# Kernel tuning notes

Hardware: AMD Instinct MI355X
Metric: run time of the kernel (lower is better)

Reference implementation:

```python
import jax, jax.numpy as jnp
import numpy as np

B, IN_DIM, D, C = 16384, 1024, 256, 100


def setup_inputs() -> dict:
    key = jax.random.key(0)
    k1, k2, k3, k4 = jax.random.split(key, 4)
    x = jax.random.normal(k1, (B, IN_DIM), dtype=jnp.float32)
    W = jax.random.normal(k2, (IN_DIM, D), dtype=jnp.float32) * (1.0 / np.sqrt(IN_DIM))
    b = jax.random.normal(k3, (D,), dtype=jnp.float32) * 0.01
    P = jax.random.normal(k4, (C, D), dtype=jnp.float32)  # class prototypes [C, D]
    return {"x": x, "W": W, "b": b, "P": P}


def reference(x, W, b, P):
    # Encoder: Z = x @ W + b  -> [B, D]
    Z = x @ W + b
    d = Z.shape[-1]
    # MSE(r, p) = mean((r - p)^2) = (|r|^2 - 2 r.p + |p|^2) / D
    # Computed via expansion to avoid the [B, C, D] broadcast intermediate.
    sq = (
        jnp.sum(Z * Z, axis=-1, keepdims=True)      # [B, 1]
        - 2.0 * (Z @ P.T)                            # [B, C]
        + jnp.sum(P * P, axis=-1)[None, :]           # [1, C]
    )
    return -sq / d  # [B, C]
```

## Files before the change

### kernel.cpp

```cpp
#include <hip/hip_runtime.h>

#define BATCH 16384
#define KDIM  1024
#define DDIM  256
#define CNUM  100
#define CPAD  112

typedef __bf16 bf16x4 __attribute__((ext_vector_type(4)));
typedef __bf16 bf16x8 __attribute__((ext_vector_type(8)));
typedef float  floatx4 __attribute__((ext_vector_type(4)));

static __device__ __forceinline__ unsigned short f2b(float f) {
    return __builtin_bit_cast(unsigned short, (__bf16)f);
}

__global__ __launch_bounds__(256) void prep_w(const float* __restrict__ W,
                                              unsigned short* __restrict__ Wt) {
    __shared__ float T[32][33];
    const int bid = blockIdx.x;
    const int k0 = (bid & 31) * 32;
    const int n0 = (bid >> 5) * 32;
    const int j  = threadIdx.x & 31;
    const int i0 = threadIdx.x >> 5;
#pragma unroll
    for (int l = 0; l < 4; ++l) {
        int i = i0 + l * 8;
        T[i][j] = W[(k0 + i) * DDIM + n0 + j];
    }
    __syncthreads();
#pragma unroll
    for (int l = 0; l < 4; ++l) {
        int i = i0 + l * 8;
        Wt[(n0 + i) * KDIM + k0 + j] = f2b(T[j][i]);
    }
}

__global__ __launch_bounds__(64) void prep_p(const float* __restrict__ P,
                                             unsigned short* __restrict__ Pbf,
                                             float* __restrict__ pnorm2) {
    const int c = blockIdx.x;
    const int lane = threadIdx.x;
    float s = 0.f;
#pragma unroll
    for (int jj = 0; jj < 4; ++jj) {
        int d = jj * 64 + lane;
        float v = (c < CNUM) ? P[c * DDIM + d] : 0.f;
        Pbf[c * DDIM + d] = f2b(v);
        s += v * v;
    }
#pragma unroll
    for (int m = 1; m < 64; m <<= 1) s += __shfl_xor(s, m, 64);
    if (lane == 0) pnorm2[c] = s;
}

__global__ __launch_bounds__(512) void fused_main(
    const float* __restrict__ x, const float* __restrict__ bias,
    const unsigned short* __restrict__ Wt, const unsigned short* __restrict__ Pbf,
    const float* __restrict__ pnorm2, float* __restrict__ out)
{
    __shared__ unsigned short As[64 * 40];
    __shared__ unsigned short Bs[256 * 40];
    __shared__ unsigned short Zs[64 * 264];
    __shared__ float rn2[2][64];

    const int tid  = threadIdx.x;
    const int wave = tid >> 6;
    const int lane = tid & 63;
    const int lm   = lane & 15;
    const int lq   = lane >> 4;
    const int rg   = wave >> 1;
    const int ch   = wave & 1;
    const int r0   = blockIdx.x * 64;

    const int rowA = tid >> 3;
    const int kcA  = (tid & 7) * 4;
    const int nB   = tid >> 1;
    const int kb0  = (tid & 1) * 16;

    const float* gA = x + (r0 + rowA) * KDIM + kcA;
    const unsigned short* gB = Wt + nB * KDIM;

    floatx4 acc[8];
#pragma unroll
    for (int f = 0; f < 8; ++f) { acc[f][0]=0.f; acc[f][1]=0.f; acc[f][2]=0.f; acc[f][3]=0.f; }

    floatx4 pa = *(const floatx4*)(gA);
    bf16x8 pb0 = *(const bf16x8*)(gB + kb0);
    bf16x8 pb1 = *(const bf16x8*)(gB + kb0 + 8);

    for (int kk = 0; kk < KDIM; kk += 32) {
        __syncthreads();
        bf16x4 ha;
        ha[0] = (__bf16)pa[0]; ha[1] = (__bf16)pa[1];
        ha[2] = (__bf16)pa[2]; ha[3] = (__bf16)pa[3];
        *(bf16x4*)&As[rowA * 40 + kcA] = ha;
        *(bf16x8*)&Bs[nB * 40 + kb0]     = pb0;
        *(bf16x8*)&Bs[nB * 40 + kb0 + 8] = pb1;
        __syncthreads();
        if (kk + 32 < KDIM) {
            pa  = *(const floatx4*)(gA + kk + 32);
            pb0 = *(const bf16x8*)(gB + kk + 32 + kb0);
            pb1 = *(const bf16x8*)(gB + kk + 32 + kb0 + 8);
        }
        bf16x8 af = *(const bf16x8*)&As[(rg * 16 + lm) * 40 + lq * 8];
#pragma unroll
        for (int f = 0; f < 8; ++f) {
            bf16x8 bfr = *(const bf16x8*)&Bs[(ch * 128 + f * 16 + lm) * 40 + lq * 8];
            acc[f] = __builtin_amdgcn_mfma_f32_16x16x32_bf16(af, bfr, acc[f], 0, 0, 0);
        }
    }

#pragma unroll
    for (int f = 0; f < 8; ++f) {
        float bb = bias[ch * 128 + f * 16 + lm];
#pragma unroll
        for (int r = 0; r < 4; ++r) acc[f][r] += bb;
    }

    float s0 = 0.f, s1 = 0.f, s2 = 0.f, s3 = 0.f;
#pragma unroll
    for (int f = 0; f < 8; ++f) {
        s0 += acc[f][0] * acc[f][0];
        s1 += acc[f][1] * acc[f][1];
        s2 += acc[f][2] * acc[f][2];
        s3 += acc[f][3] * acc[f][3];
    }
#pragma unroll
    for (int m = 1; m < 16; m <<= 1) {
        s0 += __shfl_xor(s0, m, 64);
        s1 += __shfl_xor(s1, m, 64);
        s2 += __shfl_xor(s2, m, 64);
        s3 += __shfl_xor(s3, m, 64);
    }
    if (lm == 0) {
        int rl = rg * 16 + lq * 4;
        rn2[ch][rl + 0] = s0;
        rn2[ch][rl + 1] = s1;
        rn2[ch][rl + 2] = s2;
        rn2[ch][rl + 3] = s3;
    }

#pragma unroll
    for (int f = 0; f < 8; ++f) {
        int col = ch * 128 + f * 16 + lm;
#pragma unroll
        for (int r = 0; r < 4; ++r)
            Zs[(rg * 16 + lq * 4 + r) * 264 + col] = f2b(acc[f][r]);
    }
    __syncthreads();

    if (wave < 7) {
        floatx4 acc2[4];
#pragma unroll
        for (int nf = 0; nf < 4; ++nf) { acc2[nf][0]=0.f; acc2[nf][1]=0.f; acc2[nf][2]=0.f; acc2[nf][3]=0.f; }
        const unsigned short* gP = Pbf + (wave * 16 + lm) * DDIM + lq * 8;
#pragma unroll
        for (int ks = 0; ks < 8; ++ks) {
            bf16x8 ap = *(const bf16x8*)(gP + ks * 32);
#pragma unroll
            for (int nf = 0; nf < 4; ++nf) {
                bf16x8 bz = *(const bf16x8*)&Zs[(nf * 16 + lm) * 264 + ks * 32 + lq * 8];
                acc2[nf] = __builtin_amdgcn_mfma_f32_16x16x32_bf16(ap, bz, acc2[nf], 0, 0, 0);
            }
        }
        int c0 = wave * 16 + lq * 4;
        if (c0 < CNUM) {
            floatx4 pn = *(const floatx4*)(pnorm2 + c0);
#pragma unroll
            for (int nf = 0; nf < 4; ++nf) {
                int rl = nf * 16 + lm;
                float rn = rn2[0][rl] + rn2[1][rl];
                floatx4 o;
#pragma unroll
                for (int r = 0; r < 4; ++r)
                    o[r] = (2.f * acc2[nf][r] - rn - pn[r]) * (1.f / 256.f);
                *(floatx4*)&out[(r0 + rl) * CNUM + c0] = o;
            }
        }
    }
}

extern "C" void kernel_launch(void* const* d_in, const int* in_sizes, int n_in,
                              void* d_out, int out_size, void* d_ws, size_t ws_size,
                              hipStream_t stream) {
    const float* x = (const float*)d_in[0];
    const float* W = (const float*)d_in[1];
    const float* b = (const float*)d_in[2];
    const float* P = (const float*)d_in[3];
    float* out = (float*)d_out;

    unsigned short* Wt  = (unsigned short*)d_ws;
    unsigned short* Pbf = Wt + KDIM * DDIM;
    float* pn2 = (float*)(Pbf + CPAD * DDIM);

    prep_w<<<256, 256, 0, stream>>>(W, Wt);
    prep_p<<<CPAD, 64, 0, stream>>>(P, Pbf, pn2);
    fused_main<<<BATCH / 64, 512, 0, stream>>>(x, b, Wt, Pbf, pn2, out);
}
```

Before: 136.6 us.

## Shrink row tile, load W tiles directly to LDS, alias Z buffer, merge prep kernels

Halves the rows per block to 32 with 256 threads, doubling the grid and capping launch bounds to allow more resident blocks. W tiles are now copied straight into LDS with global_load_lds instead of being staged through registers. Z aliases the A/B staging buffers to cut LDS use, and the two prep kernels are merged into one launch. The cost is that W traffic per output row doubles with the smaller tile. The unpadded 32-element LDS stride may also cause bank conflicts, and W is no longer prefetched a stage ahead.

```diff
diff --git a/kernel.cpp b/kernel.cpp
--- a/kernel.cpp
+++ b/kernel.cpp
@@ -14,54 +14,64 @@
     return __builtin_bit_cast(unsigned short, (__bf16)f);
 }
 
-__global__ __launch_bounds__(256) void prep_w(const float* __restrict__ W,
-                                              unsigned short* __restrict__ Wt) {
+static __device__ __forceinline__ void gload_lds16(const unsigned short* g,
+                                                   unsigned short* l) {
+    __builtin_amdgcn_global_load_lds(
+        (const __attribute__((address_space(1))) unsigned int*)g,
+        (__attribute__((address_space(3))) unsigned int*)l, 16, 0, 0);
+}
+
+__global__ __launch_bounds__(256) void prep(const float* __restrict__ W,
+                                            const float* __restrict__ P,
+                                            unsigned short* __restrict__ Wt,
+                                            unsigned short* __restrict__ Pbf,
+                                            float* __restrict__ pnorm2) {
     __shared__ float T[32][33];
     const int bid = blockIdx.x;
-    const int k0 = (bid & 31) * 32;
-    const int n0 = (bid >> 5) * 32;
-    const int j  = threadIdx.x & 31;
-    const int i0 = threadIdx.x >> 5;
-#pragma unroll
-    for (int l = 0; l < 4; ++l) {
-        int i = i0 + l * 8;
-        T[i][j] = W[(k0 + i) * DDIM + n0 + j];
-    }
-    __syncthreads();
-#pragma unroll
-    for (int l = 0; l < 4; ++l) {
-        int i = i0 + l * 8;
-        Wt[(n0 + i) * KDIM + k0 + j] = f2b(T[j][i]);
-    }
-}
-
-__global__ __launch_bounds__(64) void prep_p(const float* __restrict__ P,
-                                             unsigned short* __restrict__ Pbf,
-                                             float* __restrict__ pnorm2) {
-    const int c = blockIdx.x;
-    const int lane = threadIdx.x;
-    float s = 0.f;
-#pragma unroll
-    for (int jj = 0; jj < 4; ++jj) {
-        int d = jj * 64 + lane;
-        float v = (c < CNUM) ? P[c * DDIM + d] : 0.f;
-        Pbf[c * DDIM + d] = f2b(v);
-        s += v * v;
-    }
-#pragma unroll
-    for (int m = 1; m < 64; m <<= 1) s += __shfl_xor(s, m, 64);
-    if (lane == 0) pnorm2[c] = s;
-}
-
-__global__ __launch_bounds__(512) void fused_main(
+    if (bid < 256) {
+        const int k0 = (bid & 31) * 32;
+        const int n0 = (bid >> 5) * 32;
+        const int j  = threadIdx.x & 31;
+        const int i0 = threadIdx.x >> 5;
+#pragma unroll
+        for (int l = 0; l < 4; ++l) {
+            int i = i0 + l * 8;
+            T[i][j] = W[(k0 + i) * DDIM + n0 + j];
+        }
+        __syncthreads();
+#pragma unroll
+        for (int l = 0; l < 4; ++l) {
+            int i = i0 + l * 8;
+            Wt[(n0 + i) * KDIM + k0 + j] = f2b(T[j][i]);
+        }
+    } else {
+        const int wave = threadIdx.x >> 6;
+        const int lane = threadIdx.x & 63;
+        const int c = (bid - 256) * 4 + wave;
+        float s = 0.f;
+#pragma unroll
+        for (int jj = 0; jj < 4; ++jj) {
+            int d = jj * 64 + lane;
+            float v = (c < CNUM) ? P[c * DDIM + d] : 0.f;
+            Pbf[c * DDIM + d] = f2b(v);
+            s += v * v;
+        }
+#pragma unroll
+        for (int m = 1; m < 64; m <<= 1) s += __shfl_xor(s, m, 64);
+        if (lane == 0) pnorm2[c] = s;
+    }
+}
+
+__global__ __launch_bounds__(256, 8) void fused_main(
     const float* __restrict__ x, const float* __restrict__ bias,
     const unsigned short* __restrict__ Wt, const unsigned short* __restrict__ Pbf,
     const float* __restrict__ pnorm2, float* __restrict__ out)
 {
-    __shared__ unsigned short As[64 * 40];
-    __shared__ unsigned short Bs[256 * 40];
-    __shared__ unsigned short Zs[64 * 264];
-    __shared__ float rn2[2][64];
+    __shared__ unsigned short U[9216];
+    unsigned short* As = U;
+    unsigned short* Bs = U + 1024;
+    unsigned short* Zs = U;
+    __shared__ float rn2[2][32];
 
     const int tid  = threadIdx.x;
     const int wave = tid >> 6;
@@ -70,42 +80,36 @@
     const int lq   = lane >> 4;
     const int rg   = wave >> 1;
     const int ch   = wave & 1;
-    const int r0   = blockIdx.x * 64;
+    const int r0   = blockIdx.x * 32;
 
     const int rowA = tid >> 3;
     const int kcA  = (tid & 7) * 4;
-    const int nB   = tid >> 1;
-    const int kb0  = (tid & 1) * 16;
-
     const float* gA = x + (r0 + rowA) * KDIM + kcA;
-    const unsigned short* gB = Wt + nB * KDIM;
+
+    const unsigned short* gBbase = Wt + (wave * 64 + (lane >> 2)) * KDIM + (lane & 3) * 8;
 
     floatx4 acc[8];
 #pragma unroll
     for (int f = 0; f < 8; ++f) { acc[f][0]=0.f; acc[f][1]=0.f; acc[f][2]=0.f; acc[f][3]=0.f; }
 
-    floatx4 pa = *(const floatx4*)(gA);
-    bf16x8 pb0 = *(const bf16x8*)(gB + kb0);
-    bf16x8 pb1 = *(const bf16x8*)(gB + kb0 + 8);
+    floatx4 pa = *(const floatx4*)gA;
 
     for (int kk = 0; kk < KDIM; kk += 32) {
         __syncthreads();
+#pragma unroll
+        for (int c = 0; c < 4; ++c)
+            gload_lds16(gBbase + (c * 16) * KDIM + kk, Bs + (wave * 4 + c) * 512);
         bf16x4 ha;
         ha[0] = (__bf16)pa[0]; ha[1] = (__bf16)pa[1];
         ha[2] = (__bf16)pa[2]; ha[3] = (__bf16)pa[3];
-        *(bf16x4*)&As[rowA * 40 + kcA] = ha;
-        *(bf16x8*)&Bs[nB * 40 + kb0]     = pb0;
-        *(bf16x8*)&Bs[nB * 40 + kb0 + 8] = pb1;
+        *(bf16x4*)&As[rowA * 32 + kcA] = ha;
         __syncthreads();
-        if (kk + 32 < KDIM) {
-            pa  = *(const floatx4*)(gA + kk + 32);
-            pb0 = *(const bf16x8*)(gB + kk + 32 + kb0);
-            pb1 = *(const bf16x8*)(gB + kk + 32 + kb0 + 8);
-        }
-        bf16x8 af = *(const bf16x8*)&As[(rg * 16 + lm) * 40 + lq * 8];
+        bf16x8 af = *(const bf16x8*)&As[(rg * 16 + lm) * 32 + lq * 8];
+        if (kk + 32 < KDIM)
+            pa = *(const floatx4*)(gA + kk + 32);
 #pragma unroll
         for (int f = 0; f < 8; ++f) {
-            bf16x8 bfr = *(const bf16x8*)&Bs[(ch * 128 + f * 16 + lm) * 40 + lq * 8];
+            bf16x8 bfr = *(const bf16x8*)&Bs[(ch * 128 + f * 16 + lm) * 32 + lq * 8];
             acc[f] = __builtin_amdgcn_mfma_f32_16x16x32_bf16(af, bfr, acc[f], 0, 0, 0);
         }
     }
@@ -140,6 +144,8 @@
         rn2[ch][rl + 3] = s3;
     }
 
+    __syncthreads();
+
 #pragma unroll
     for (int f = 0; f < 8; ++f) {
         int col = ch * 128 + f * 16 + lm;
@@ -149,32 +155,36 @@
     }
     __syncthreads();
 
-    if (wave < 7) {
-        floatx4 acc2[4];
-#pragma unroll
-        for (int nf = 0; nf < 4; ++nf) { acc2[nf][0]=0.f; acc2[nf][1]=0.f; acc2[nf][2]=0.f; acc2[nf][3]=0.f; }
-        const unsigned short* gP = Pbf + (wave * 16 + lm) * DDIM + lq * 8;
-#pragma unroll
-        for (int ks = 0; ks < 8; ++ks) {
-            bf16x8 ap = *(const bf16x8*)(gP + ks * 32);
-#pragma unroll
-            for (int nf = 0; nf < 4; ++nf) {
-                bf16x8 bz = *(const bf16x8*)&Zs[(nf * 16 + lm) * 264 + ks * 32 + lq * 8];
-                acc2[nf] = __builtin_amdgcn_mfma_f32_16x16x32_bf16(ap, bz, acc2[nf], 0, 0, 0);
+#pragma unroll
+    for (int t = 0; t < 2; ++t) {
+        const int ct = wave * 2 + t;
+        if (ct < 7) {
+            floatx4 acc2[2];
+#pragma unroll
+            for (int nf = 0; nf < 2; ++nf) { acc2[nf][0]=0.f; acc2[nf][1]=0.f; acc2[nf][2]=0.f; acc2[nf][3]=0.f; }
+            const unsigned short* gP = Pbf + (ct * 16 + lm) * DDIM + lq * 8;
+#pragma unroll
+            for (int ks = 0; ks < 8; ++ks) {
+                bf16x8 ap = *(const bf16x8*)(gP + ks * 32);
+#pragma unroll
+                for (int nf = 0; nf < 2; ++nf) {
+                    bf16x8 bz = *(const bf16x8*)&Zs[(nf * 16 + lm) * 264 + ks * 32 + lq * 8];
+                    acc2[nf] = __builtin_amdgcn_mfma_f32_16x16x32_bf16(ap, bz, acc2[nf], 0, 0, 0);
+                }
             }
-        }
-        int c0 = wave * 16 + lq * 4;
-        if (c0 < CNUM) {
-            floatx4 pn = *(const floatx4*)(pnorm2 + c0);
-#pragma unroll
-            for (int nf = 0; nf < 4; ++nf) {
-                int rl = nf * 16 + lm;
-                float rn = rn2[0][rl] + rn2[1][rl];
-                floatx4 o;
-#pragma unroll
-                for (int r = 0; r < 4; ++r)
-                    o[r] = (2.f * acc2[nf][r] - rn - pn[r]) * (1.f / 256.f);
-                *(floatx4*)&out[(r0 + rl) * CNUM + c0] = o;
+            int c0 = ct * 16 + lq * 4;
+            if (c0 < CNUM) {
+                floatx4 pn = *(const floatx4*)(pnorm2 + c0);
+#pragma unroll
+                for (int nf = 0; nf < 2; ++nf) {
+                    int rl = nf * 16 + lm;
+                    float rn = rn2[0][rl] + rn2[1][rl];
+                    floatx4 o;
+#pragma unroll
+                    for (int r = 0; r < 4; ++r)
+                        o[r] = (2.f * acc2[nf][r] - rn - pn[r]) * (1.f / 256.f);
+                    *(floatx4*)&out[(r0 + rl) * CNUM + c0] = o;
+                }
             }
         }
     }
@@ -193,7 +203,6 @@
     unsigned short* Pbf = Wt + KDIM * DDIM;
     float* pn2 = (float*)(Pbf + CPAD * DDIM);
 
-    prep_w<<<256, 256, 0, stream>>>(W, Wt);
-    prep_p<<<CPAD, 64, 0, stream>>>(P, Pbf, pn2);
-    fused_main<<<BATCH / 64, 512, 0, stream>>>(x, b, Wt, Pbf, pn2, out);
-}
+    prep<<<256 + CPAD / 4, 256, 0, stream>>>(W, P, Wt, Pbf, pn2);
+    fused_main<<<BATCH / 32, 256, 0, stream>>>(x, b, Wt, Pbf, pn2, out);
+}
```

Result: no change. 134.1 us (-1.8%).

## Load GEMM operands directly into registers, widen block to 16 waves, merge prep kernels

Applied to the files above, without the earlier changes.

The first GEMM no longer stages x and Wt tiles through shared memory. Each wave loads its MFMA fragments straight from global memory into registers with one-step prefetching, which removes two barriers per k-step. The block grows to 1024 threads (16 waves, each covering a 16x64 output tile), and the row-norm reduction now sums four partials. The two prep kernels are merged into one launch. In exchange, Wt fragments are reread by every block without LDS reuse, global loads become narrow strided 16-byte accesses, and large blocks may limit occupancy.

```diff
diff --git a/kernel.cpp b/kernel.cpp
--- a/kernel.cpp
+++ b/kernel.cpp
@@ -14,112 +14,112 @@
     return __builtin_bit_cast(unsigned short, (__bf16)f);
 }
 
-__global__ __launch_bounds__(256) void prep_w(const float* __restrict__ W,
-                                              unsigned short* __restrict__ Wt) {
+__global__ __launch_bounds__(256) void prep(const float* __restrict__ W,
+                                            const float* __restrict__ P,
+                                            unsigned short* __restrict__ Wt,
+                                            unsigned short* __restrict__ Pbf,
+                                            float* __restrict__ pnorm2) {
     __shared__ float T[32][33];
     const int bid = blockIdx.x;
-    const int k0 = (bid & 31) * 32;
-    const int n0 = (bid >> 5) * 32;
-    const int j  = threadIdx.x & 31;
-    const int i0 = threadIdx.x >> 5;
+    if (bid < 256) {
+        const int k0 = (bid & 31) * 32;
+        const int n0 = (bid >> 5) * 32;
+        const int j  = threadIdx.x & 31;
+        const int i0 = threadIdx.x >> 5;
 #pragma unroll
-    for (int l = 0; l < 4; ++l) {
-        int i = i0 + l * 8;
-        T[i][j] = W[(k0 + i) * DDIM + n0 + j];
-    }
-    __syncthreads();
+        for (int l = 0; l < 4; ++l) {
+            int i = i0 + l * 8;
+            T[i][j] = W[(k0 + i) * DDIM + n0 + j];
+        }
+        __syncthreads();
 #pragma unroll
-    for (int l = 0; l < 4; ++l) {
-        int i = i0 + l * 8;
-        Wt[(n0 + i) * KDIM + k0 + j] = f2b(T[j][i]);
+        for (int l = 0; l < 4; ++l) {
+            int i = i0 + l * 8;
+            Wt[(n0 + i) * KDIM + k0 + j] = f2b(T[j][i]);
+        }
+    } else {
+        const int wave = threadIdx.x >> 6;
+        const int lane = threadIdx.x & 63;
+        const int c = (bid - 256) * 4 + wave;
+        float s = 0.f;
+#pragma unroll
+        for (int jj = 0; jj < 4; ++jj) {
+            int d = jj * 64 + lane;
+            float v = (c < CNUM) ? P[c * DDIM + d] : 0.f;
+            Pbf[c * DDIM + d] = f2b(v);
+            s += v * v;
+        }
+#pragma unroll
+        for (int m = 1; m < 64; m <<= 1) s += __shfl_xor(s, m, 64);
+        if (lane == 0) pnorm2[c] = s;
     }
 }
 
-__global__ __launch_bounds__(64) void prep_p(const float* __restrict__ P,
-                                             unsigned short* __restrict__ Pbf,
-                                             float* __restrict__ pnorm2) {
-    const int c = blockIdx.x;
-    const int lane = threadIdx.x;
-    float s = 0.f;
-#pragma unroll
-    for (int jj = 0; jj < 4; ++jj) {
-        int d = jj * 64 + lane;
-        float v = (c < CNUM) ? P[c * DDIM + d] : 0.f;
-        Pbf[c * DDIM + d] = f2b(v);
-        s += v * v;
-    }
-#pragma unroll
-    for (int m = 1; m < 64; m <<= 1) s += __shfl_xor(s, m, 64);
-    if (lane == 0) pnorm2[c] = s;
-}
-
-__global__ __launch_bounds__(512) void fused_main(
+__global__ __launch_bounds__(1024, 4) void fused_main(
     const float* __restrict__ x, const float* __restrict__ bias,
     const unsigned short* __restrict__ Wt, const unsigned short* __restrict__ Pbf,
     const float* __restrict__ pnorm2, float* __restrict__ out)
 {
-    __shared__ unsigned short As[64 * 40];
-    __shared__ unsigned short Bs[256 * 40];
     __shared__ unsigned short Zs[64 * 264];
-    __shared__ float rn2[2][64];
+    __shared__ float rn2[4][64];
 
     const int tid  = threadIdx.x;
     const int wave = tid >> 6;
     const int lane = tid & 63;
     const int lm   = lane & 15;
     const int lq   = lane >> 4;
-    const int rg   = wave >> 1;
-    const int ch   = wave & 1;
+    const int rc   = wave & 3;
+    const int cc   = wave >> 2;
     const int r0   = blockIdx.x * 64;
 
-    const int rowA = tid >> 3;
-    const int kcA  = (tid & 7) * 4;
-    const int nB   = tid >> 1;
-    const int kb0  = (tid & 1) * 16;
+    const float* gA = x + (r0 + rc * 16 + lm) * KDIM + lq * 8;
+    const unsigned short* gB = Wt + (cc * 64 + lm) * KDIM + lq * 8;
 
-    const float* gA = x + (r0 + rowA) * KDIM + kcA;
-    const unsigned short* gB = Wt + nB * KDIM;
+    floatx4 acc[4];
+#pragma unroll
+    for (int f = 0; f < 4; ++f) { acc[f][0]=0.f; acc[f][1]=0.f; acc[f][2]=0.f; acc[f][3]=0.f; }
 
-    floatx4 acc[8];
+    floatx4 a0 = *(const floatx4*)(gA);
+    floatx4 a1 = *(const floatx4*)(gA + 4);
+    bf16x8 bfr[4];
 #pragma unroll
-    for (int f = 0; f < 8; ++f) { acc[f][0]=0.f; acc[f][1]=0.f; acc[f][2]=0.f; acc[f][3]=0.f; }
+    for (int f = 0; f < 4; ++f)
+        bfr[f] = *(const bf16x8*)(gB + f * 16 * KDIM);
 
-    floatx4 pa = *(const floatx4*)(gA);
-    bf16x8 pb0 = *(const bf16x8*)(gB + kb0);
-    bf16x8 pb1 = *(const bf16x8*)(gB + kb0 + 8);
-
+#pragma unroll 2
     for (int kk = 0; kk < KDIM; kk += 32) {
-        __syncthreads();
-        bf16x4 ha;
-        ha[0] = (__bf16)pa[0]; ha[1] = (__bf16)pa[1];
-        ha[2] = (__bf16)pa[2]; ha[3] = (__bf16)pa[3];
-        *(bf16x4*)&As[rowA * 40 + kcA] = ha;
-        *(bf16x8*)&Bs[nB * 40 + kb0]     = pb0;
-        *(bf16x8*)&Bs[nB * 40 + kb0 + 8] = pb1;
-        __syncthreads();
+        floatx4 na0, na1;
+        bf16x8 nb[4];
         if (kk + 32 < KDIM) {
-            pa  = *(const floatx4*)(gA + kk + 32);
-            pb0 = *(const bf16x8*)(gB + kk + 32 + kb0);
-            pb1 = *(const bf16x8*)(gB + kk + 32 + kb0 + 8);
+            na0 = *(const floatx4*)(gA + kk + 32);
+            na1 = *(const floatx4*)(gA + kk + 36);
+#pragma unroll
+            for (int f = 0; f < 4; ++f)
+                nb[f] = *(const bf16x8*)(gB + f * 16 * KDIM + kk + 32);
         }
-        bf16x8 af = *(const bf16x8*)&As[(rg * 16 + lm) * 40 + lq * 8];
+        bf16x8 af;
+        af[0] = (__bf16)a0[0]; af[1] = (__bf16)a0[1];
+        af[2] = (__bf16)a0[2]; af[3] = (__bf16)a0[3];
+        af[4] = (__bf16)a1[0]; af[5] = (__bf16)a1[1];
+        af[6] = (__bf16)a1[2]; af[7] = (__bf16)a1[3];
 #pragma unroll
-        for (int f = 0; f < 8; ++f) {
-            bf16x8 bfr = *(const bf16x8*)&Bs[(ch * 128 + f * 16 + lm) * 40 + lq * 8];
-            acc[f] = __builtin_amdgcn_mfma_f32_16x16x32_bf16(af, bfr, acc[f], 0, 0, 0);
-        }
+        for (int f = 0; f < 4; ++f)
+            acc[f] = __builtin_amdgcn_mfma_f32_16x16x32_bf16(af, bfr[f], acc[f], 0, 0, 0);
+        a0 = na0; a1 = na1;
+#pragma unroll
+        for (int f = 0; f < 4; ++f) bfr[f] = nb[f];
     }
 
 #pragma unroll
-    for (int f = 0; f < 8; ++f) {
-        float bb = bias[ch * 128 + f * 16 + lm];
+    for (int f = 0; f < 4; ++f) {
+        float bb = bias[cc * 64 + f * 16 + lm];
 #pragma unroll
         for (int r = 0; r < 4; ++r) acc[f][r] += bb;
     }
 
     float s0 = 0.f, s1 = 0.f, s2 = 0.f, s3 = 0.f;
 #pragma unroll
-    for (int f = 0; f < 8; ++f) {
+    for (int f = 0; f < 4; ++f) {
         s0 += acc[f][0] * acc[f][0];
         s1 += acc[f][1] * acc[f][1];
         s2 += acc[f][2] * acc[f][2];
@@ -133,19 +133,19 @@
         s3 += __shfl_xor(s3, m, 64);
     }
     if (lm == 0) {
-        int rl = rg * 16 + lq * 4;
-        rn2[ch][rl + 0] = s0;
-        rn2[ch][rl + 1] = s1;
-        rn2[ch][rl + 2] = s2;
-        rn2[ch][rl + 3] = s3;
+        int rl = rc * 16 + lq * 4;
+        rn2[cc][rl + 0] = s0;
+        rn2[cc][rl + 1] = s1;
+        rn2[cc][rl + 2] = s2;
+        rn2[cc][rl + 3] = s3;
     }
 
 #pragma unroll
-    for (int f = 0; f < 8; ++f) {
-        int col = ch * 128 + f * 16 + lm;
+    for (int f = 0; f < 4; ++f) {
+        int col = cc * 64 + f * 16 + lm;
 #pragma unroll
         for (int r = 0; r < 4; ++r)
-            Zs[(rg * 16 + lq * 4 + r) * 264 + col] = f2b(acc[f][r]);
+            Zs[(rc * 16 + lq * 4 + r) * 264 + col] = f2b(acc[f][r]);
     }
     __syncthreads();
 
@@ -169,7 +169,7 @@
 #pragma unroll
             for (int nf = 0; nf < 4; ++nf) {
                 int rl = nf * 16 + lm;
-                float rn = rn2[0][rl] + rn2[1][rl];
+                float rn = rn2[0][rl] + rn2[1][rl] + rn2[2][rl] + rn2[3][rl];
                 floatx4 o;
 #pragma unroll
                 for (int r = 0; r < 4; ++r)
@@ -193,7 +193,6 @@
     unsigned short* Pbf = Wt + KDIM * DDIM;
     float* pn2 = (float*)(Pbf + CPAD * DDIM);
 
-    prep_w<<<256, 256, 0, stream>>>(W, Wt);
-    prep_p<<<CPAD, 64, 0, stream>>>(P, Pbf, pn2);
-    fused_main<<<BATCH / 64, 512, 0, stream>>>(x, b, Wt, Pbf, pn2, out);
+    prep<<<256 + CPAD / 4, 256, 0, stream>>>(W, P, Wt, Pbf, pn2);
+    fused_main<<<BATCH / 64, 1024, 0, stream>>>(x, b, Wt, Pbf, pn2, out);
 }
```

New measurement: 179.6 us. 1.31x slower.
